# Kernel tuning notes

Hardware: AMD Instinct MI355X
Metric: run time of the kernel (lower is better)

The kernel has to match this reference:

```python
import jax, jax.numpy as jnp
import numpy as np
from jax import lax

B, H, W, C, G, K = 2, 64, 64, 256, 8, 9
CQ = C // 4  # PConv partial channels
HC = C // G  # head channels
PTS = np.array([[-1, -1], [-1, 0], [-1, 1], [0, -1], [0, 0], [0, 1],
                [1, -1], [1, 0], [1, 1]], np.float32)  # (K,2) as (dx,dy)


def setup_inputs() -> dict:
    key = jax.random.key(0)
    ks = jax.random.split(key, 13)
    n = lambda i, shp, s: jax.random.normal(ks[i], shp, jnp.float32) * s
    return {
        'x': jax.random.normal(ks[0], (B, H, W, C), jnp.float32),
        'qkv_w': n(1, (C, 3 * C), C ** -0.5),
        'qkv_b': n(2, (3 * C,), 0.02),
        'dw_w': n(3, (3, 3, 1, 3 * C), 1.0 / 3.0),
        'dw_b': n(4, (3 * C,), 0.02),
        'off_pconv_w': n(5, (G, CQ, CQ, 3, 3), (CQ * 9) ** -0.5),
        'off_w': n(6, (G, 2 * K, C), 0.1 * C ** -0.5),
        'off_b': n(7, (G, 2 * K), 0.1),
        'mask_pconv_w': n(8, (CQ, CQ, 3, 3), (CQ * 9) ** -0.5),
        'mask_w': n(9, (K, C), C ** -0.5),
        'mask_b': n(10, (K,), 0.02),
        'proj_w': n(11, (C, C), C ** -0.5),
        'proj_b': n(12, (C,), 0.02),
    }


def _dwconv_nhwc(x, w, b):
    # depthwise 3x3, pad 1, stride 1; x (B,H,W,ch), w (3,3,1,ch)
    ch = x.shape[-1]
    y = lax.conv_general_dilated(x, w, (1, 1), 'SAME',
                                 dimension_numbers=('NHWC', 'HWIO', 'NHWC'),
                                 feature_group_count=ch)
    return y + b


def _pconv_nchw(x, w):
    # partial conv: 3x3 (no bias) on first CQ channels, rest untouched
    dc = w.shape[0]
    x1 = lax.conv_general_dilated(x[:, :dc], w, (1, 1), 'SAME',
                                  dimension_numbers=('NCHW', 'OIHW', 'NCHW'))
    return jnp.concatenate([x1, x[:, dc:]], axis=1)


def _flow_warp(x, flow):
    # x (N,Cc,Hh,Ww), flow (N,2K,Hh,Ww) -> (N,Cc,K,Hh,Ww)
    # bilinear grid_sample, border padding, align_corners=True == sampling at
    # absolute pixel coords with coordinate clamping.
    N, Cc, Hh, Ww = x.shape
    Kk = flow.shape[1] // 2
    fl = flow.reshape(N, Kk, 2, Hh, Ww).transpose(0, 3, 4, 1, 2)  # (N,H,W,K,2)
    gy, gx = jnp.meshgrid(jnp.arange(Hh, dtype=x.dtype),
                          jnp.arange(Ww, dtype=x.dtype), indexing='ij')
    base = jnp.stack([gx, gy], axis=-1)  # (H,W,2) in (x,y) order
    coords = base[None, :, :, None, :] + fl  # (N,H,W,K,2)
    cx = jnp.clip(coords[..., 0], 0.0, Ww - 1)
    cy = jnp.clip(coords[..., 1], 0.0, Hh - 1)
    x0 = jnp.floor(cx)
    y0 = jnp.floor(cy)
    wx = (cx - x0).reshape(N, 1, -1)
    wy = (cy - y0).reshape(N, 1, -1)
    x0i = x0.astype(jnp.int32)
    y0i = y0.astype(jnp.int32)
    x1i = jnp.minimum(x0i + 1, Ww - 1)
    y1i = jnp.minimum(y0i + 1, Hh - 1)
    xf = x.reshape(N, Cc, Hh * Ww)

    def gather(yi, xi):
        idx = (yi * Ww + xi).reshape(N, -1)  # (N, H*W*K)
        return jax.vmap(lambda im, ix: im[:, ix])(xf, idx)  # (N,Cc,H*W*K)

    v00 = gather(y0i, x0i)
    v01 = gather(y0i, x1i)
    v10 = gather(y1i, x0i)
    v11 = gather(y1i, x1i)
    out = (v00 * (1 - wx) * (1 - wy) + v01 * wx * (1 - wy)
           + v10 * (1 - wx) * wy + v11 * wx * wy)
    return out.reshape(N, Cc, Hh, Ww, Kk).transpose(0, 1, 4, 2, 3)


def reference(x, qkv_w, qkv_b, dw_w, dw_b, off_pconv_w, off_w, off_b,
              mask_pconv_w, mask_w, mask_b, proj_w, proj_b):
    Bb, Hh, Ww, Cc = x.shape
    P = Hh * Ww
    scale = HC ** -0.5
    # qkv projection + depthwise conv (NHWC)
    qkv = x @ qkv_w + qkv_b                       # (B,H,W,3C)
    qkv = _dwconv_nhwc(qkv, dw_w, dw_b)
    q = qkv[..., :Cc]                             # (B,H,W,C)
    k_map = jnp.transpose(qkv[..., Cc:2 * Cc], (0, 3, 1, 2))   # (B,C,H,W)
    v_map = jnp.transpose(qkv[..., 2 * Cc:], (0, 3, 1, 2))     # (B,C,H,W)
    q_nchw = jnp.transpose(q, (0, 3, 1, 2))

    # shared mask conv: PConv + 1x1 -> (B,K,H,W)
    xm = _pconv_nchw(q_nchw, mask_pconv_w)
    mask = jnp.einsum('bchw,oc->bohw', xm, mask_w) + mask_b[None, :, None, None]

    # base offsets per group: points_pool * (2g+1), flattened (dx,dy) pairs
    base = jnp.asarray(np.stack([(PTS * (2 * g + 1)).reshape(-1)
                                 for g in range(G)], axis=0))  # (G,2K)

    k_list, v_list = [], []
    for g in range(G):
        xo = _pconv_nchw(q_nchw, off_pconv_w[g])
        off = (jnp.einsum('bchw,oc->bohw', xo, off_w[g])
               + off_b[g][None, :, None, None]
               + base[g][None, :, None, None])  # (B,2K,H,W)
        sl = slice(g * HC, (g + 1) * HC)
        k_list.append(_flow_warp(k_map[:, sl], off) * mask[:, None])
        v_list.append(_flow_warp(v_map[:, sl], off) * mask[:, None])

    # stack (G,B,hc,K,H,W) -> (B,G,P,K,hc)
    def arrange(lst):
        t = jnp.stack(lst, axis=0).transpose(1, 0, 4, 5, 3, 2)
        return t.reshape(Bb, G, P, K, HC)

    k = arrange(k_list)
    v = arrange(v_list)
    qh = (q.reshape(Bb, Hh, Ww, G, HC).transpose(0, 3, 1, 2, 4)
          .reshape(Bb, G, P, HC)) * scale

    attn = jnp.einsum('bgpc,bgpkc->bgpk', qh, k)
    attn = jax.nn.softmax(attn, axis=-1)
    out = jnp.einsum('bgpk,bgpkc->bgpc', attn, v)       # (B,G,P,hc)
    out = out.transpose(0, 2, 1, 3).reshape(Bb, Hh, Ww, Cc)
    return out @ proj_w + proj_b
```

## Files before the change

kernel.cpp:

```cpp
#include <hip/hip_runtime.h>

typedef unsigned short u16;
typedef unsigned int u32;
typedef short bf16x8 __attribute__((ext_vector_type(8)));
typedef float f32x4 __attribute__((ext_vector_type(4)));
typedef float f32x2 __attribute__((ext_vector_type(2)));
typedef u32 u32x2 __attribute__((ext_vector_type(2)));

#define PP 4096
#define KPT 9

__device__ __forceinline__ u16 f2b(float f) {
    union { float f; unsigned int u; } v; v.f = f;
    unsigned int u = v.u;
    unsigned int r = u + 0x7FFFu + ((u >> 16) & 1u);
    return (u16)(r >> 16);
}
__device__ __forceinline__ float b2f(u16 b) {
    union { unsigned int u; float f; } v; v.u = ((unsigned int)b) << 16;
    return v.f;
}
__device__ __forceinline__ f32x2 unpk2(u32 u) {
    f32x2 r;
    r.x = __uint_as_float(u << 16);
    r.y = __uint_as_float(u & 0xFFFF0000u);
    return r;
}

__global__ __launch_bounds__(256) void prep_weights(
        const float* __restrict__ qkv_w, const float* __restrict__ proj_w,
        const float* __restrict__ off_pconv_w, const float* __restrict__ off_w,
        const float* __restrict__ off_b, const float* __restrict__ mask_pconv_w,
        const float* __restrict__ mask_w, const float* __restrict__ mask_b,
        u16* __restrict__ qkv_wT_b, u16* __restrict__ proj_wT_b,
        u16* __restrict__ cwT_b, float* __restrict__ cb) {
    int blk = blockIdx.x;
    if (blk < 1024) {
        int idx = blk * 256 + threadIdx.x;
        if (idx < 196608) {
            int r = idx / 768, c = idx % 768;
            qkv_wT_b[c * 256 + r] = f2b(qkv_w[idx]);
        } else {
            int i3 = idx - 196608;
            int r = i3 >> 8, c = i3 & 255;
            proj_wT_b[c * 256 + r] = f2b(proj_w[i3]);
        }
        return;
    }
    int k = blk - 1024;
    int o = threadIdx.x;
    if (o >= 160) return;
    float val = 0.f;
    if (o < 153) {
        if (k < 576) {
            int patch = k >> 6, i = k & 63;
            if (o < 144) {
                int g = o / 18, oo = o % 18;
                for (int c = 0; c < 64; c++)
                    val += off_w[(g * 18 + oo) * 256 + c] *
                           off_pconv_w[((g * 64 + c) * 64 + i) * 9 + patch];
            } else {
                int oo = o - 144;
                for (int c = 0; c < 64; c++)
                    val += mask_w[oo * 256 + c] * mask_pconv_w[(c * 64 + i) * 9 + patch];
            }
        } else {
            int j = k - 576;
            if (o < 144) {
                int g = o / 18, oo = o % 18;
                val = off_w[(g * 18 + oo) * 256 + 64 + j];
            } else {
                val = mask_w[(o - 144) * 256 + 64 + j];
            }
        }
    }
    cwT_b[o * 768 + k] = f2b(val);
    if (k == 0) {
        float bv = 0.f;
        if (o < 144) {
            int g = o / 18, oo = o % 18;
            const float PTSf[18] = {-1,-1,-1,0,-1,1,0,-1,0,0,0,1,1,-1,1,0,1,1};
            bv = off_b[g * 18 + oo] + PTSf[oo] * (float)(2 * g + 1);
        } else if (o < 153) {
            bv = mask_b[o - 144];
        }
        cb[o] = bv;
    }
}

template<bool OUT_BF16, bool A_F32, int KD>
__global__ __launch_bounds__(256) void mfma_gemm(
        const void* __restrict__ Av, const u16* __restrict__ BT,
        const float* __restrict__ bias, void* __restrict__ out, int N) {
    __shared__ u16 As[64][40];
    __shared__ u16 Bs[64][40];
    int tid = threadIdx.x;
    int row0 = blockIdx.x * 64, col0 = blockIdx.y * 64;
    int wid = tid >> 6, lane = tid & 63;
    int wr = wid >> 1, wc = wid & 1;
    int l15 = lane & 15, lhi = lane >> 4;
    f32x4 acc[2][2] = {};
    #pragma unroll
    for (int k0 = 0; k0 < KD; k0 += 32) {
        {
            int r = tid >> 2, kc = (tid & 3) * 8;
            if (A_F32) {
                const float* Af = (const float*)Av;
                f32x4 a0 = *(const f32x4*)&Af[(size_t)(row0 + r) * KD + k0 + kc];
                f32x4 a1 = *(const f32x4*)&Af[(size_t)(row0 + r) * KD + k0 + kc + 4];
                bf16x8 v;
                #pragma unroll
                for (int j = 0; j < 4; j++) { v[j] = (short)f2b(a0[j]); v[4+j] = (short)f2b(a1[j]); }
                *(bf16x8*)&As[r][kc] = v;
            } else {
                const u16* Ab = (const u16*)Av;
                *(bf16x8*)&As[r][kc] = *(const bf16x8*)&Ab[(size_t)(row0 + r) * KD + k0 + kc];
            }
            *(bf16x8*)&Bs[r][kc] = *(const bf16x8*)&BT[(size_t)(col0 + r) * KD + k0 + kc];
        }
        __syncthreads();
        bf16x8 bfr[2], afr[2];
        #pragma unroll
        for (int j = 0; j < 2; j++) {
            bfr[j] = *(const bf16x8*)&Bs[wc * 32 + j * 16 + l15][lhi * 8];
            afr[j] = *(const bf16x8*)&As[wr * 32 + j * 16 + l15][lhi * 8];
        }
        #pragma unroll
        for (int i = 0; i < 2; i++)
            #pragma unroll
            for (int j = 0; j < 2; j++)
                acc[i][j] = __builtin_amdgcn_mfma_f32_16x16x32_bf16(afr[i], bfr[j], acc[i][j], 0, 0, 0);
        __syncthreads();
    }
    #pragma unroll
    for (int i = 0; i < 2; i++) {
        int row = row0 + wr * 32 + i * 16 + lhi * 4;
        #pragma unroll
        for (int j = 0; j < 2; j++) {
            int col = col0 + wc * 32 + j * 16 + l15;
            float bv = bias[col];
            #pragma unroll
            for (int r = 0; r < 4; r++) {
                float v = acc[i][j][r] + bv;
                if (OUT_BF16) ((u16*)out)[(size_t)(row + r) * N + col] = f2b(v);
                else          ((float*)out)[(size_t)(row + r) * N + col] = v;
            }
        }
    }
}

__global__ __launch_bounds__(256) void dwconv_b(const u16* __restrict__ qkv_b,
        const float* __restrict__ dww, const float* __restrict__ dwb,
        u16* __restrict__ out) {
    int idx = blockIdx.x * 256 + threadIdx.x;
    int c8 = (idx % 96) * 8;
    int pix = idx / 96;
    int w = pix & 63, h = (pix >> 6) & 63, b = pix >> 12;
    float acc[8];
    #pragma unroll
    for (int j = 0; j < 8; j++) acc[j] = dwb[c8 + j];
    #pragma unroll
    for (int ky = 0; ky < 3; ky++) {
        int hh = h + ky - 1;
        if (hh < 0 || hh >= 64) continue;
        #pragma unroll
        for (int kx = 0; kx < 3; kx++) {
            int ww = w + kx - 1;
            if (ww < 0 || ww >= 64) continue;
            bf16x8 v = *(const bf16x8*)&qkv_b[((size_t)((b * 64 + hh) * 64 + ww)) * 768 + c8];
            #pragma unroll
            for (int j = 0; j < 8; j++)
                acc[j] += b2f((u16)v[j]) * dww[(ky * 3 + kx) * 768 + c8 + j];
        }
    }
    bf16x8 o;
    #pragma unroll
    for (int j = 0; j < 8; j++) o[j] = (short)f2b(acc[j]);
    *(bf16x8*)&out[(size_t)idx * 8] = o;
}

__global__ __launch_bounds__(256) void offmask_mfma(const u16* __restrict__ qdw_b,
        const u16* __restrict__ cwT_b, const float* __restrict__ cb,
        float* __restrict__ om0, float* __restrict__ om1) {
    __shared__ u16 As[32][40];
    __shared__ u16 Bs[160][40];
    int tid = threadIdx.x;
    int half = blockIdx.x & 1;
    int p0 = (blockIdx.x >> 1) * 32;
    int kbeg = half ? 384 : 0;
    int kend = kbeg + 384;
    int wid = tid >> 6, lane = tid & 63;
    int wr = wid >> 1, wc = wid & 1;
    int l15 = lane & 15, lhi = lane >> 4;
    f32x4 acc[5] = {};
    for (int k0 = kbeg; k0 < kend; k0 += 32) {
        if (tid < 128) {
            int r = tid >> 2, kc = (tid & 3) * 8;
            int pixel = p0 + r;
            int w = pixel & 63, h = (pixel >> 6) & 63, b = pixel >> 12;
            bf16x8 v = {};
            if (k0 < 576) {
                int patch = k0 >> 6;
                int dy = patch / 3 - 1, dx = patch % 3 - 1;
                int hh = h + dy, ww = w + dx;
                if (hh >= 0 && hh < 64 && ww >= 0 && ww < 64)
                    v = *(const bf16x8*)&qdw_b[((size_t)((b * 64 + hh) * 64 + ww)) * 768 + (k0 & 63) + kc];
            } else {
                v = *(const bf16x8*)&qdw_b[((size_t)((b * 64 + h) * 64 + w)) * 768 + 64 + (k0 - 576) + kc];
            }
            *(bf16x8*)&As[r][kc] = v;
        }
        for (int idx = tid; idx < 640; idx += 256) {
            int r = idx >> 2, kc = (idx & 3) * 8;
            *(bf16x8*)&Bs[r][kc] = *(const bf16x8*)&cwT_b[r * 768 + k0 + kc];
        }
        __syncthreads();
        bf16x8 afr = *(const bf16x8*)&As[wr * 16 + l15][lhi * 8];
        #pragma unroll
        for (int j = 0; j < 5; j++) {
            bf16x8 bfr = *(const bf16x8*)&Bs[wc * 80 + j * 16 + l15][lhi * 8];
            acc[j] = __builtin_amdgcn_mfma_f32_16x16x32_bf16(afr, bfr, acc[j], 0, 0, 0);
        }
        __syncthreads();
    }
    float* dst = half ? om1 : om0;
    int row = p0 + wr * 16 + lhi * 4;
    #pragma unroll
    for (int j = 0; j < 5; j++) {
        int col = wc * 80 + j * 16 + l15;
        float bv = half ? 0.f : cb[col];
        #pragma unroll
        for (int r = 0; r < 4; r++)
            dst[(size_t)(row + r) * 160 + col] = acc[j][r] + bv;
    }
}

__global__ __launch_bounds__(256) void precompute_pts(const float* __restrict__ om0,
        const float* __restrict__ om1, float4* __restrict__ pre) {
    int idx = blockIdx.x * 256 + threadIdx.x;
    if (idx >= 2 * PP * 72) return;
    int item = idx % 72;
    int pix = idx / 72;
    int g = item / 9, k = item % 9;
    int w = pix & 63, h = (pix >> 6) & 63;
    size_t rowb = (size_t)pix * 160;
    float dx = om0[rowb + g * 18 + 2 * k]     + om1[rowb + g * 18 + 2 * k];
    float dy = om0[rowb + g * 18 + 2 * k + 1] + om1[rowb + g * 18 + 2 * k + 1];
    float m  = om0[rowb + 144 + k]            + om1[rowb + 144 + k];
    float cx = fminf(fmaxf((float)w + dx, 0.f), 63.f);
    float cy = fminf(fmaxf((float)h + dy, 0.f), 63.f);
    float x0f = floorf(cx), y0f = floorf(cy);
    int x0 = (int)x0f, y0 = (int)y0f;
    u32 idx00 = (u32)((pix & ~4095) | (y0 << 6) | x0);
    u32 pk = idx00 | ((x0 < 63) ? 0x10000u : 0u) | ((y0 < 63) ? 0x20000u : 0u);
    float4 o;
    o.x = __uint_as_float(pk);
    o.y = cx - x0f;
    o.z = cy - y0f;
    o.w = m;
    pre[idx] = o;
}

__global__ __launch_bounds__(256) void deform_attn(const u16* __restrict__ qdw_b,
        const float4* __restrict__ pre, u16* __restrict__ attn_b) {
    int tid = threadIdx.x;
    int bid = blockIdx.x;
    int sbid = (bid & 7) * 256 + (bid >> 3);
    int t = tid >> 3;
    int cl = tid & 7;
    int g = t & 7;
    int pix = sbid * 4 + (t >> 3);
    const float scale = 0.17677669529663687f;
    int c0 = g * 32 + 4 * cl;
    u32x2 qu = *(const u32x2*)&qdw_b[(size_t)pix * 768 + c0];
    f32x2 qa = unpk2(qu.x) * scale;
    f32x2 qb = unpk2(qu.y) * scale;
    const float4* pp = pre + (size_t)pix * 72 + g * 9;
    const char* base = (const char*)qdw_b;
    u32 ckb = (u32)(512 + c0 * 2);
    float logit[KPT];
    f32x2 va[KPT], vb[KPT];
    #pragma unroll
    for (int k_ = 0; k_ < KPT; k_++) {
        float4 q4 = pp[k_];
        u32 pk = __float_as_uint(q4.x);
        float wx = q4.y, wy = q4.z, m = q4.w;
        u32 o00 = (pk & 0xFFFFu) * 1536u + ckb;
        u32 dX = (pk & 0x10000u) ? 1536u : 0u;
        u32 dY = (pk & 0x20000u) ? 98304u : 0u;
        u32 o01 = o00 + dX, o10 = o00 + dY, o11 = o00 + dY + dX;
        u32x2 K00 = *(const u32x2*)(base + o00);
        u32x2 V00 = *(const u32x2*)(base + o00 + 512);
        u32x2 K01 = *(const u32x2*)(base + o01);
        u32x2 V01 = *(const u32x2*)(base + o01 + 512);
        u32x2 K10 = *(const u32x2*)(base + o10);
        u32x2 V10 = *(const u32x2*)(base + o10 + 512);
        u32x2 K11 = *(const u32x2*)(base + o11);
        u32x2 V11 = *(const u32x2*)(base + o11 + 512);
        float w00 = (1.f - wx) * (1.f - wy), w01 = wx * (1.f - wy);
        float w10 = (1.f - wx) * wy,         w11 = wx * wy;
        f32x2 ka = unpk2(K00.x) * w00 + unpk2(K01.x) * w01
                 + unpk2(K10.x) * w10 + unpk2(K11.x) * w11;
        f32x2 kb = unpk2(K00.y) * w00 + unpk2(K01.y) * w01
                 + unpk2(K10.y) * w10 + unpk2(K11.y) * w11;
        f32x2 vva = unpk2(V00.x) * w00 + unpk2(V01.x) * w01
                  + unpk2(V10.x) * w10 + unpk2(V11.x) * w11;
        f32x2 vvb = unpk2(V00.y) * w00 + unpk2(V01.y) * w01
                  + unpk2(V10.y) * w10 + unpk2(V11.y) * w11;
        f32x2 pr = qa * ka + qb * kb;
        float part = pr.x + pr.y;
        part += __shfl_xor(part, 4);
        part += __shfl_xor(part, 2);
        part += __shfl_xor(part, 1);
        logit[k_] = part * m;
        va[k_] = vva * m;
        vb[k_] = vvb * m;
    }
    float mx = fmaxf(fmaxf(fmaxf(logit[0], logit[1]), fmaxf(logit[2], logit[3])),
                     fmaxf(fmaxf(logit[4], logit[5]),
                           fmaxf(fmaxf(logit[6], logit[7]), logit[8])));
    float s = 0.f;
    #pragma unroll
    for (int k_ = 0; k_ < KPT; k_++) { logit[k_] = __expf(logit[k_] - mx); s += logit[k_]; }
    float inv = 1.f / s;
    f32x2 oa = {0.f, 0.f}, ob = {0.f, 0.f};
    #pragma unroll
    for (int k_ = 0; k_ < KPT; k_++) { oa += va[k_] * logit[k_]; ob += vb[k_] * logit[k_]; }
    oa *= inv; ob *= inv;
    u32x2 outw;
    outw.x = (u32)f2b(oa.x) | ((u32)f2b(oa.y) << 16);
    outw.y = (u32)f2b(ob.x) | ((u32)f2b(ob.y) << 16);
    *(u32x2*)&attn_b[(size_t)pix * 256 + c0] = outw;
}

extern "C" void kernel_launch(void* const* d_in, const int* in_sizes, int n_in,
                              void* d_out, int out_size, void* d_ws, size_t ws_size,
                              hipStream_t stream) {
    const float* x            = (const float*)d_in[0];
    const float* qkv_w        = (const float*)d_in[1];
    const float* qkv_b        = (const float*)d_in[2];
    const float* dw_w         = (const float*)d_in[3];
    const float* dw_b         = (const float*)d_in[4];
    const float* off_pconv_w  = (const float*)d_in[5];
    const float* off_w        = (const float*)d_in[6];
    const float* off_b        = (const float*)d_in[7];
    const float* mask_pconv_w = (const float*)d_in[8];
    const float* mask_w       = (const float*)d_in[9];
    const float* mask_b       = (const float*)d_in[10];
    const float* proj_w       = (const float*)d_in[11];
    const float* proj_b       = (const float*)d_in[12];

    char* ws = (char*)d_ws;
    size_t off = 0;
    u16*   qkv_wT_b   = (u16*)(ws + off);                 off += 768ull*256*2;
    u16*   proj_wT_b  = (u16*)(ws + off);                 off += 256ull*256*2;
    u16*   qkv_bf     = (u16*)(ws + off);                 off += 8192ull*768*2;
    u16*   qdw_b      = (u16*)(ws + off);                 off += 8192ull*768*2;
    u16*   cwT_b      = (u16*)(ws + off);                 off += 160ull*768*2;
    float* cb         = (float*)(ws + off);               off += 256*4;
    float* om0        = (float*)(ws + off);               off += 8192ull*160*4;
    float* om1        = (float*)(ws + off);               off += 8192ull*160*4;
    u16*   attn_b     = (u16*)(ws + off);                 off += 8192ull*256*2;
    float4* pre       = (float4*)(ws + off);              off += 589824ull*16;

    prep_weights<<<1792, 256, 0, stream>>>(qkv_w, proj_w, off_pconv_w, off_w, off_b,
                                           mask_pconv_w, mask_w, mask_b,
                                           qkv_wT_b, proj_wT_b, cwT_b, cb);
    mfma_gemm<true, true, 256><<<dim3(128, 12), 256, 0, stream>>>(x, qkv_wT_b, qkv_b,
                                                                  qkv_bf, 768);
    dwconv_b<<<3072, 256, 0, stream>>>(qkv_bf, dw_w, dw_b, qdw_b);
    offmask_mfma<<<512, 256, 0, stream>>>(qdw_b, cwT_b, cb, om0, om1);
    precompute_pts<<<2304, 256, 0, stream>>>(om0, om1, pre);
    deform_attn<<<2048, 256, 0, stream>>>(qdw_b, pre, attn_b);
    mfma_gemm<false, false, 256><<<dim3(128, 4), 256, 0, stream>>>(attn_b, proj_wT_b,
                                                                   proj_b, d_out, 256);
}
```

Before: 171.8 us.

## Fuse sample-point precompute into deform_attn and split offmask K four ways

The standalone precompute_pts kernel is removed. Each deform_attn block now computes the bilinear sample parameters for its 4 pixels into shared memory, which drops one launch and the write and re-read of the float4 parameter buffer. The offset/mask GEMM's reduction is split into four K chunks instead of two, doubling the block count for more parallelism. The cost is four partial-sum buffers that deform_attn must read and add, plus a block-wide sync before sampling.

```diff
diff --git a/kernel.cpp b/kernel.cpp
--- a/kernel.cpp
+++ b/kernel.cpp
@@ -181,14 +181,15 @@
 
 __global__ __launch_bounds__(256) void offmask_mfma(const u16* __restrict__ qdw_b,
         const u16* __restrict__ cwT_b, const float* __restrict__ cb,
-        float* __restrict__ om0, float* __restrict__ om1) {
+        float* __restrict__ om0, float* __restrict__ om1,
+        float* __restrict__ om2, float* __restrict__ om3) {
     __shared__ u16 As[32][40];
     __shared__ u16 Bs[160][40];
     int tid = threadIdx.x;
-    int half = blockIdx.x & 1;
-    int p0 = (blockIdx.x >> 1) * 32;
-    int kbeg = half ? 384 : 0;
-    int kend = kbeg + 384;
+    int half = blockIdx.x & 3;
+    int p0 = (blockIdx.x >> 2) * 32;
+    int kbeg = half * 192;
+    int kend = kbeg + 192;
     int wid = tid >> 6, lane = tid & 63;
     int wr = wid >> 1, wc = wid & 1;
     int l15 = lane & 15, lhi = lane >> 4;
@@ -223,49 +224,60 @@
         }
         __syncthreads();
     }
-    float* dst = half ? om1 : om0;
+    float* dst = (half == 0) ? om0 : (half == 1) ? om1 : (half == 2) ? om2 : om3;
     int row = p0 + wr * 16 + lhi * 4;
     #pragma unroll
     for (int j = 0; j < 5; j++) {
         int col = wc * 80 + j * 16 + l15;
-        float bv = half ? 0.f : cb[col];
+        float bv = (half == 0) ? cb[col] : 0.f;
         #pragma unroll
         for (int r = 0; r < 4; r++)
             dst[(size_t)(row + r) * 160 + col] = acc[j][r] + bv;
     }
 }
 
-__global__ __launch_bounds__(256) void precompute_pts(const float* __restrict__ om0,
-        const float* __restrict__ om1, float4* __restrict__ pre) {
-    int idx = blockIdx.x * 256 + threadIdx.x;
-    if (idx >= 2 * PP * 72) return;
-    int item = idx % 72;
-    int pix = idx / 72;
-    int g = item / 9, k = item % 9;
+__device__ __forceinline__ float4 pt_params(const float* __restrict__ om0,
+        const float* __restrict__ om1, const float* __restrict__ om2,
+        const float* __restrict__ om3, int pix, int g, int k) {
     int w = pix & 63, h = (pix >> 6) & 63;
     size_t rowb = (size_t)pix * 160;
-    float dx = om0[rowb + g * 18 + 2 * k]     + om1[rowb + g * 18 + 2 * k];
-    float dy = om0[rowb + g * 18 + 2 * k + 1] + om1[rowb + g * 18 + 2 * k + 1];
-    float m  = om0[rowb + 144 + k]            + om1[rowb + 144 + k];
+    size_t db = rowb + g * 18 + 2 * k;
+    f32x2 d0 = *(const f32x2*)&om0[db];
+    f32x2 d1 = *(const f32x2*)&om1[db];
+    f32x2 d2 = *(const f32x2*)&om2[db];
+    f32x2 d3 = *(const f32x2*)&om3[db];
+    float m = om0[rowb + 144 + k] + om1[rowb + 144 + k]
+            + om2[rowb + 144 + k] + om3[rowb + 144 + k];
+    float dx = d0.x + d1.x + d2.x + d3.x;
+    float dy = d0.y + d1.y + d2.y + d3.y;
     float cx = fminf(fmaxf((float)w + dx, 0.f), 63.f);
     float cy = fminf(fmaxf((float)h + dy, 0.f), 63.f);
     float x0f = floorf(cx), y0f = floorf(cy);
     int x0 = (int)x0f, y0 = (int)y0f;
-    u32 idx00 = (u32)((pix & ~4095) | (y0 << 6) | x0);
-    u32 pk = idx00 | ((x0 < 63) ? 0x10000u : 0u) | ((y0 < 63) ? 0x20000u : 0u);
+    u32 pk = (u32)((pix & ~4095) | (y0 << 6) | x0)
+           | ((x0 < 63) ? 0x10000u : 0u) | ((y0 < 63) ? 0x20000u : 0u);
     float4 o;
     o.x = __uint_as_float(pk);
     o.y = cx - x0f;
     o.z = cy - y0f;
     o.w = m;
-    pre[idx] = o;
+    return o;
 }
 
 __global__ __launch_bounds__(256) void deform_attn(const u16* __restrict__ qdw_b,
-        const float4* __restrict__ pre, u16* __restrict__ attn_b) {
+        const float* __restrict__ om0, const float* __restrict__ om1,
+        const float* __restrict__ om2, const float* __restrict__ om3,
+        u16* __restrict__ attn_b) {
+    __shared__ float4 ptp[288];
     int tid = threadIdx.x;
     int bid = blockIdx.x;
     int sbid = (bid & 7) * 256 + (bid >> 3);
+    for (int j = tid; j < 288; j += 256) {
+        int u = j / 9, k = j % 9;
+        int ppix = sbid * 4 + (u >> 3);
+        ptp[j] = pt_params(om0, om1, om2, om3, ppix, u & 7, k);
+    }
+    __syncthreads();
     int t = tid >> 3;
     int cl = tid & 7;
     int g = t & 7;
@@ -275,14 +287,13 @@
     u32x2 qu = *(const u32x2*)&qdw_b[(size_t)pix * 768 + c0];
     f32x2 qa = unpk2(qu.x) * scale;
     f32x2 qb = unpk2(qu.y) * scale;
-    const float4* pp = pre + (size_t)pix * 72 + g * 9;
     const char* base = (const char*)qdw_b;
     u32 ckb = (u32)(512 + c0 * 2);
     float logit[KPT];
     f32x2 va[KPT], vb[KPT];
     #pragma unroll
     for (int k_ = 0; k_ < KPT; k_++) {
-        float4 q4 = pp[k_];
+        float4 q4 = ptp[t * 9 + k_];
         u32 pk = __float_as_uint(q4.x);
         float wx = q4.y, wy = q4.z, m = q4.w;
         u32 o00 = (pk & 0xFFFFu) * 1536u + ckb;
@@ -360,8 +371,9 @@
     float* cb         = (float*)(ws + off);               off += 256*4;
     float* om0        = (float*)(ws + off);               off += 8192ull*160*4;
     float* om1        = (float*)(ws + off);               off += 8192ull*160*4;
+    float* om2        = (float*)(ws + off);               off += 8192ull*160*4;
+    float* om3        = (float*)(ws + off);               off += 8192ull*160*4;
     u16*   attn_b     = (u16*)(ws + off);                 off += 8192ull*256*2;
-    float4* pre       = (float4*)(ws + off);              off += 589824ull*16;
 
     prep_weights<<<1792, 256, 0, stream>>>(qkv_w, proj_w, off_pconv_w, off_w, off_b,
                                            mask_pconv_w, mask_w, mask_b,
@@ -369,9 +381,8 @@
     mfma_gemm<true, true, 256><<<dim3(128, 12), 256, 0, stream>>>(x, qkv_wT_b, qkv_b,
                                                                   qkv_bf, 768);
     dwconv_b<<<3072, 256, 0, stream>>>(qkv_bf, dw_w, dw_b, qdw_b);
-    offmask_mfma<<<512, 256, 0, stream>>>(qdw_b, cwT_b, cb, om0, om1);
-    precompute_pts<<<2304, 256, 0, stream>>>(om0, om1, pre);
-    deform_attn<<<2048, 256, 0, stream>>>(qdw_b, pre, attn_b);
+    offmask_mfma<<<1024, 256, 0, stream>>>(qdw_b, cwT_b, cb, om0, om1, om2, om3);
+    deform_attn<<<2048, 256, 0, stream>>>(qdw_b, om0, om1, om2, om3, attn_b);
     mfma_gemm<false, false, 256><<<dim3(128, 4), 256, 0, stream>>>(attn_b, proj_wT_b,
                                                                    proj_b, d_out, 256);
 }
```

After: 162.8 us. 1.06x faster.
